# Kernel optimization log

Measured on AMD Instinct MI355X. Metric: run time of the kernel, lower is better.

The kernel has to match this reference:

```python
import jax, jax.numpy as jnp
import numpy as np

B, L, C = 131072, 50, 3
WIN = 10  # running std window


def setup_inputs() -> dict:
    key = jax.random.key(0)
    ks = jax.random.split(key, 12)
    def xavier(k, shape, fan_in, fan_out, gain):
        bound = gain * np.sqrt(6.0 / (fan_in + fan_out))
        return jax.random.uniform(k, shape, jnp.float32, -bound, bound)
    relu_g = np.sqrt(2.0)
    return {
        "signal": jax.random.normal(ks[0], (B, L, C), jnp.float32),
        # conv weights: (out_ch, in_ch, kernel)
        "conv1_w": xavier(ks[1], (5, 3, 3), 3 * 3, 5 * 3, relu_g),
        "conv1_b": jnp.zeros((5,), jnp.float32),
        "conv2_w": xavier(ks[2], (10, 5, 3), 5 * 3, 10 * 3, relu_g),
        "conv2_b": jnp.zeros((10,), jnp.float32),
        "fc1_w": xavier(ks[3], (256, 360), 360, 256, relu_g),
        "fc1_b": jnp.zeros((256,), jnp.float32),
        "fc2_w": xavier(ks[4], (64, 256), 256, 64, relu_g),
        "fc2_b": jnp.zeros((64,), jnp.float32),
        "pamap_w": xavier(ks[5], (12, 64), 64, 12, 1.0),
        "pamap_b": jnp.zeros((12,), jnp.float32),
    }


def running_std(x, w):
    # x: (B, L, C) -> (B, L - w, C); unbiased std (ddof=1) over sliding window,
    # computed with prefix sums instead of per-window kernels.
    b, l, c = x.shape
    z = jnp.zeros((b, 1, c), x.dtype)
    cs = jnp.concatenate([z, jnp.cumsum(x, axis=1)], axis=1)
    cs2 = jnp.concatenate([z, jnp.cumsum(x * x, axis=1)], axis=1)
    lo = l - w  # note: torch loop produces L - w windows (last window dropped)
    s = cs[:, w:w + lo] - cs[:, :lo]
    s2 = cs2[:, w:w + lo] - cs2[:, :lo]
    var = (s2 - s * s / w) / (w - 1)
    return jnp.sqrt(jnp.maximum(var, 0.0))


def conv1d(x, w, b):
    # x: (B, C, T), w: (O, I, K)
    y = jax.lax.conv_general_dilated(x, w, (1,), 'VALID',
                                     dimension_numbers=('NCH', 'OIH', 'NCH'))
    return y + b[None, :, None]


def reference(signal, conv1_w, conv1_b, conv2_w, conv2_b,
              fc1_w, fc1_b, fc2_w, fc2_b, pamap_w, pamap_b):
    sd = running_std(signal, WIN)            # (B, 40, 3)
    x = jnp.transpose(sd, (0, 2, 1))          # (B, 3, 40)
    h = jax.nn.relu(conv1d(x, conv1_w, conv1_b))   # (B, 5, 38)
    h = jax.nn.relu(conv1d(h, conv2_w, conv2_b))   # (B, 10, 36)
    flat = jnp.transpose(h, (0, 2, 1)).reshape(-1, 36 * 10)  # (B, 360)
    f = jax.nn.relu(flat @ fc1_w.T + fc1_b)
    f = jax.nn.relu(f @ fc2_w.T + fc2_b)
    logits = f @ pamap_w.T + pamap_b           # flag=False -> pamap head
    return jax.nn.log_softmax(logits, axis=1)
```

## Files before the change

kernel.cpp:

```cpp
#include <hip/hip_runtime.h>
#include <hip/hip_bf16.h>

typedef __attribute__((ext_vector_type(8))) short bf16x8;
typedef __attribute__((ext_vector_type(4))) float f32x4;
typedef __attribute__((ext_vector_type(8))) unsigned short u16x8;

static __device__ __forceinline__ unsigned short bf16bits(float v) {
    __hip_bfloat16 h = __float2bfloat16(v);
    return *(unsigned short*)&h;
}

__global__ __launch_bounds__(256) void prep_weights(
    const float* __restrict__ fc1w, const float* __restrict__ fc2w,
    __hip_bfloat16* __restrict__ w1o, __hip_bfloat16* __restrict__ w2o)
{
    int id = blockIdx.x * 256 + threadIdx.x;
    if (id < 256 * 384) {
        int n = id / 384, k2 = id - n * 384;
        float v = 0.0f;
        if (k2 < 360) {
            int o = k2 / 36, t = k2 - o * 36;
            v = fc1w[n * 360 + t * 10 + o];
        }
        w1o[id] = __float2bfloat16(v);
    } else {
        int id2 = id - 256 * 384;
        if (id2 < 64 * 256) w2o[id2] = __float2bfloat16(fc2w[id2]);
    }
}

__global__ __launch_bounds__(256, 8) void features_kernel(
    const float* __restrict__ sig,
    const float* __restrict__ c1w_g, const float* __restrict__ c1b_g,
    const float* __restrict__ c2w_g, const float* __restrict__ c2b_g,
    __hip_bfloat16* __restrict__ Fg)
{
    __shared__ __align__(16) unsigned char smem[16648];
    float* Sraw = (float*)smem;
    float* SD   = (float*)(smem + 4800);
    float* C1   = (float*)(smem + 9408);
    float* cw   = (float*)(smem + 15808);

    const int tid = threadIdx.x;
    const int blk = blockIdx.x;

    {
        const float4* gs = (const float4*)(sig + (size_t)blk * 1200);
        float4* ls = (float4*)Sraw;
        for (int i = tid; i < 300; i += 256) ls[i] = gs[i];
        if (tid < 210) {
            float v;
            if (tid < 45)       v = c1w_g[tid];
            else if (tid < 50)  v = c1b_g[tid - 45];
            else if (tid < 200) v = c2w_g[tid - 50];
            else                v = c2b_g[tid - 200];
            cw[tid] = v;
        }
    }
    __syncthreads();

    if (tid < 192) {
        int s = tid / 24, r = tid - s * 24;
        int c = r >> 3, q = r & 7;
        const float* p = Sraw + s * 150 + c + q * 15;
        float x[14];
        #pragma unroll
        for (int j = 0; j < 14; ++j) x[j] = p[j * 3];
        float sum = 0.f, sq = 0.f;
        #pragma unroll
        for (int j = 0; j < 10; ++j) { sum += x[j]; sq += x[j] * x[j]; }
        float* o = SD + (s * 3 + c) * 48 + q * 5;
        #pragma unroll
        for (int i = 0; i < 5; ++i) {
            float var = (sq - sum * sum * 0.1f) * (1.0f / 9.0f);
            o[i] = sqrtf(fmaxf(var, 0.f));
            if (i < 4) {
                float d = x[i + 10] - x[i];
                sq  += d * (x[i + 10] + x[i]);
                sum += d;
            }
        }
    }
    __syncthreads();

    for (int id = tid; id < 400; id += 256) {
        int s = id / 50, r = id - s * 50;
        int o = r / 10, tq = r - o * 10;
        int t0 = tq * 4;
        float b = cw[45 + o];
        float a0 = b, a1 = b, a2 = b, a3 = b;
        #pragma unroll
        for (int ci = 0; ci < 3; ++ci) {
            const float* row = SD + (s * 3 + ci) * 48 + t0;
            float4 ya = *(const float4*)row;
            float4 yb = *(const float4*)(row + 4);
            float w0 = cw[o * 9 + ci * 3 + 0];
            float w1 = cw[o * 9 + ci * 3 + 1];
            float w2 = cw[o * 9 + ci * 3 + 2];
            a0 += w0 * ya.x + w1 * ya.y + w2 * ya.z;
            a1 += w0 * ya.y + w1 * ya.z + w2 * ya.w;
            a2 += w0 * ya.z + w1 * ya.w + w2 * yb.x;
            a3 += w0 * ya.w + w1 * yb.x + w2 * yb.y;
        }
        float* dst = C1 + (s * 5 + o) * 40 + t0;
        if (tq < 9) {
            float4 v = {fmaxf(a0, 0.f), fmaxf(a1, 0.f), fmaxf(a2, 0.f), fmaxf(a3, 0.f)};
            *(float4*)dst = v;
        } else {
            dst[0] = fmaxf(a0, 0.f);
            dst[1] = fmaxf(a1, 0.f);
        }
    }
    __syncthreads();

    if (tid < 96) {
        int s = tid / 12, j = tid - s * 12;
        *(unsigned int*)(smem + s * 768 + 720 + 4 * j) = 0u;
    }
    for (int id = tid; id < 720; id += 256) {
        int s = id / 90, r = id - s * 90;
        int o = r / 9, tq = r - o * 9;
        int t0 = tq * 4;
        float b = cw[200 + o];
        float a0 = b, a1 = b, a2 = b, a3 = b;
        #pragma unroll
        for (int i2 = 0; i2 < 5; ++i2) {
            const float* row = C1 + (s * 5 + i2) * 40 + t0;
            float4 ya = *(const float4*)row;
            float4 yb = *(const float4*)(row + 4);
            float w0 = cw[50 + o * 15 + i2 * 3 + 0];
            float w1 = cw[50 + o * 15 + i2 * 3 + 1];
            float w2 = cw[50 + o * 15 + i2 * 3 + 2];
            a0 += w0 * ya.x + w1 * ya.y + w2 * ya.z;
            a1 += w0 * ya.y + w1 * ya.z + w2 * ya.w;
            a2 += w0 * ya.z + w1 * ya.w + w2 * yb.x;
            a3 += w0 * ya.w + w1 * yb.x + w2 * yb.y;
        }
        unsigned int p0 = (unsigned int)bf16bits(fmaxf(a0, 0.f))
                        | ((unsigned int)bf16bits(fmaxf(a1, 0.f)) << 16);
        unsigned int p1 = (unsigned int)bf16bits(fmaxf(a2, 0.f))
                        | ((unsigned int)bf16bits(fmaxf(a3, 0.f)) << 16);
        uint2 pk = {p0, p1};
        *(uint2*)(smem + s * 768 + (o * 36 + t0) * 2) = pk;
    }
    __syncthreads();

    {
        const u16x8* srcv = (const u16x8*)smem;
        u16x8* dstv = (u16x8*)Fg + (size_t)blk * 384;
        for (int i = tid; i < 384; i += 256) dstv[i] = srcv[i];
    }
}

__global__ __launch_bounds__(256, 2) void fc_head_kernel(
    const __hip_bfloat16* __restrict__ Fg,
    const __hip_bfloat16* __restrict__ W1, const __hip_bfloat16* __restrict__ W2,
    const float* __restrict__ fc1b, const float* __restrict__ fc2b,
    const float* __restrict__ pw, const float* __restrict__ pb,
    float* __restrict__ out)
{
    __shared__ __align__(16) unsigned char smem[63536];
    float* pwl = (float*)(smem + 60416);
    float* pbl = (float*)(smem + 63488);

    const int tid  = threadIdx.x;
    const int blk  = blockIdx.x;
    const int w    = tid >> 6;
    const int lane = tid & 63;
    const int ml   = lane & 15;
    const int kg   = lane >> 4;
    unsigned char* Tw = smem + 50176 + w * 2560;

    for (int i = tid; i < 780; i += 256) {
        if (i < 768) pwl[i] = pw[i]; else pbl[i - 768] = pb[i - 768];
    }

    const __hip_bfloat16* myF = Fg + (size_t)(blk * 128 + w * 32 + ml) * 384;
    bf16x8 bfr[12][2];
    #pragma unroll
    for (int kk = 0; kk < 12; ++kk) {
        bfr[kk][0] = *(const bf16x8*)(myF + kk * 32 + kg * 8);
        bfr[kk][1] = *(const bf16x8*)(myF + 16 * 384 + kk * 32 + kg * 8);
    }

    {
        const u16x8* src = (const u16x8*)W1;
        __hip_bfloat16* b0 = (__hip_bfloat16*)smem;
        #pragma unroll
        for (int it = 0; it < 6; ++it) {
            int v = tid + it * 256;
            int n = v / 48, k8 = v - n * 48;
            *(u16x8*)(b0 + n * 392 + k8 * 8) = src[v];
        }
    }

    f32x4 acc2[4][2];
    #pragma unroll
    for (int t2 = 0; t2 < 4; ++t2) {
        acc2[t2][0] = f32x4{0, 0, 0, 0};
        acc2[t2][1] = f32x4{0, 0, 0, 0};
    }

    for (int c = 0; c < 8; ++c) {
        __syncthreads();
        const __hip_bfloat16* cur = (const __hip_bfloat16*)(smem + (c & 1) * 25088);

        u16x8 nf[6];
        if (c < 7) {
            const u16x8* src = (const u16x8*)(W1 + (c + 1) * 32 * 384);
            #pragma unroll
            for (int it = 0; it < 6; ++it) nf[it] = src[tid + it * 256];
        }

        f32x4 a1acc[2][2];
        #pragma unroll
        for (int rt = 0; rt < 2; ++rt) {
            a1acc[rt][0] = f32x4{0, 0, 0, 0};
            a1acc[rt][1] = f32x4{0, 0, 0, 0};
        }
        #pragma unroll
        for (int kk = 0; kk < 12; ++kk) {
            bf16x8 w0 = *(const bf16x8*)(cur + ml * 392 + kk * 32 + kg * 8);
            bf16x8 w1 = *(const bf16x8*)(cur + (16 + ml) * 392 + kk * 32 + kg * 8);
            a1acc[0][0] = __builtin_amdgcn_mfma_f32_16x16x32_bf16(w0, bfr[kk][0], a1acc[0][0], 0, 0, 0);
            a1acc[0][1] = __builtin_amdgcn_mfma_f32_16x16x32_bf16(w0, bfr[kk][1], a1acc[0][1], 0, 0, 0);
            a1acc[1][0] = __builtin_amdgcn_mfma_f32_16x16x32_bf16(w1, bfr[kk][0], a1acc[1][0], 0, 0, 0);
            a1acc[1][1] = __builtin_amdgcn_mfma_f32_16x16x32_bf16(w1, bfr[kk][1], a1acc[1][1], 0, 0, 0);
        }

        #pragma unroll
        for (int rt = 0; rt < 2; ++rt) {
            float4 b4 = *(const float4*)(fc1b + c * 32 + rt * 16 + kg * 4);
            #pragma unroll
            for (int st = 0; st < 2; ++st) {
                unsigned int p0 =
                    (unsigned int)bf16bits(fmaxf(a1acc[rt][st][0] + b4.x, 0.f))
                  | ((unsigned int)bf16bits(fmaxf(a1acc[rt][st][1] + b4.y, 0.f)) << 16);
                unsigned int p1 =
                    (unsigned int)bf16bits(fmaxf(a1acc[rt][st][2] + b4.z, 0.f))
                  | ((unsigned int)bf16bits(fmaxf(a1acc[rt][st][3] + b4.w, 0.f)) << 16);
                uint2 pk = {p0, p1};
                *(uint2*)(Tw + (st * 16 + ml) * 80 + (rt * 16 + kg * 4) * 2) = pk;
            }
        }
        asm volatile("s_waitcnt lgkmcnt(0)" ::: "memory");
        __builtin_amdgcn_sched_barrier(0);

        bf16x8 pf0 = *(const bf16x8*)(Tw + ml * 80 + kg * 16);
        bf16x8 pf1 = *(const bf16x8*)(Tw + (16 + ml) * 80 + kg * 16);
        #pragma unroll
        for (int t2 = 0; t2 < 4; ++t2) {
            bf16x8 a2 = *(const bf16x8*)(W2 + (t2 * 16 + ml) * 256 + c * 32 + kg * 8);
            acc2[t2][0] = __builtin_amdgcn_mfma_f32_16x16x32_bf16(a2, pf0, acc2[t2][0], 0, 0, 0);
            acc2[t2][1] = __builtin_amdgcn_mfma_f32_16x16x32_bf16(a2, pf1, acc2[t2][1], 0, 0, 0);
        }

        if (c < 7) {
            __hip_bfloat16* nxt = (__hip_bfloat16*)(smem + ((c + 1) & 1) * 25088);
            #pragma unroll
            for (int it = 0; it < 6; ++it) {
                int v = tid + it * 256;
                int n = v / 48, k8 = v - n * 48;
                *(u16x8*)(nxt + n * 392 + k8 * 8) = nf[it];
            }
        }
    }

    #pragma unroll
    for (int st = 0; st < 2; ++st) {
        float h[16];
        #pragma unroll
        for (int t2 = 0; t2 < 4; ++t2) {
            float4 b4 = *(const float4*)(fc2b + t2 * 16 + kg * 4);
            #pragma unroll
            for (int i = 0; i < 4; ++i)
                h[t2 * 4 + i] = fmaxf(acc2[t2][st][i] + ((const float*)&b4)[i], 0.f);
        }
        float lg[12];
        #pragma unroll
        for (int j = 0; j < 12; ++j) {
            float s = 0.f;
            #pragma unroll
            for (int t2 = 0; t2 < 4; ++t2) {
                float4 wv = *(const float4*)(pwl + j * 64 + t2 * 16 + kg * 4);
                s += wv.x * h[t2 * 4 + 0] + wv.y * h[t2 * 4 + 1]
                   + wv.z * h[t2 * 4 + 2] + wv.w * h[t2 * 4 + 3];
            }
            lg[j] = s;
        }
        #pragma unroll
        for (int j = 0; j < 12; ++j) {
            lg[j] += __shfl_xor(lg[j], 16);
            lg[j] += __shfl_xor(lg[j], 32);
            lg[j] += pbl[j];
        }
        float m = lg[0];
        #pragma unroll
        for (int j = 1; j < 12; ++j) m = fmaxf(m, lg[j]);
        float e = 0.f;
        #pragma unroll
        for (int j = 0; j < 12; ++j) e += __expf(lg[j] - m);
        float lse = m + __logf(e);
        if (kg == 0) {
            float* op = out + (size_t)(blk * 128 + w * 32 + st * 16 + ml) * 12;
            float4 o0 = {lg[0] - lse, lg[1] - lse, lg[2]  - lse, lg[3]  - lse};
            float4 o1 = {lg[4] - lse, lg[5] - lse, lg[6]  - lse, lg[7]  - lse};
            float4 o2 = {lg[8] - lse, lg[9] - lse, lg[10] - lse, lg[11] - lse};
            ((float4*)op)[0] = o0; ((float4*)op)[1] = o1; ((float4*)op)[2] = o2;
        }
    }
}

extern "C" void kernel_launch(void* const* d_in, const int* in_sizes, int n_in,
                              void* d_out, int out_size, void* d_ws, size_t ws_size,
                              hipStream_t stream) {
    const float* sig = (const float*)d_in[0];
    const float* c1w = (const float*)d_in[1];
    const float* c1b = (const float*)d_in[2];
    const float* c2w = (const float*)d_in[3];
    const float* c2b = (const float*)d_in[4];
    const float* f1w = (const float*)d_in[5];
    const float* f1b = (const float*)d_in[6];
    const float* f2w = (const float*)d_in[7];
    const float* f2b = (const float*)d_in[8];
    const float* pw  = (const float*)d_in[9];
    const float* pb  = (const float*)d_in[10];
    float* out = (float*)d_out;

    __hip_bfloat16* W1 = (__hip_bfloat16*)d_ws;
    __hip_bfloat16* W2 = (__hip_bfloat16*)((char*)d_ws + 196608);
    __hip_bfloat16* Fg = (__hip_bfloat16*)((char*)d_ws + 229376);

    prep_weights<<<448, 256, 0, stream>>>(f1w, f2w, W1, W2);
    features_kernel<<<16384, 256, 0, stream>>>(sig, c1w, c1b, c2w, c2b, Fg);
    fc_head_kernel<<<1024, 256, 0, stream>>>(Fg, W1, W2, f1b, f2b, pw, pb, out);
}
```

Measured before the change: 245.2 us.

## Run conv layers on MFMA with 32 samples per block; prefetch W2 fragments

The features kernel now handles 32 samples per block instead of 8. It reads the signal straight from global memory into registers to compute the running std, stores it as bf16, and computes both conv1d layers as im2col-style 16x16x32 bf16 MFMAs with padded shared-memory tiles. This replaces the scalar FMA loops. The fc head also prefetches the next W2 A-fragments into registers one chunk ahead. The gains come from removing scalar conv work and raising per-block throughput. The costs are lower occupancy from larger LDS, uncoalesced strided global reads of the signal, and bf16 rounding of the intermediate features.

```diff
diff --git a/kernel.cpp b/kernel.cpp
--- a/kernel.cpp
+++ b/kernel.cpp
@@ -29,25 +29,35 @@
     }
 }
 
-__global__ __launch_bounds__(256, 8) void features_kernel(
+#define P_BASE  0
+#define P_TILE  10496
+#define P_SSTR  656
+#define SD_BASE 20992
+#define SD_TILE 11008
+#define SD_SSTR 688
+#define F_BASE  20992
+#define F_RSTR  784
+#define CW_OFF  46080
+__global__ __launch_bounds__(256, 3) void features_kernel(
     const float* __restrict__ sig,
     const float* __restrict__ c1w_g, const float* __restrict__ c1b_g,
     const float* __restrict__ c2w_g, const float* __restrict__ c2b_g,
     __hip_bfloat16* __restrict__ Fg)
 {
-    __shared__ __align__(16) unsigned char smem[16648];
-    float* Sraw = (float*)smem;
-    float* SD   = (float*)(smem + 4800);
-    float* C1   = (float*)(smem + 9408);
-    float* cw   = (float*)(smem + 15808);
-
-    const int tid = threadIdx.x;
-    const int blk = blockIdx.x;
-
-    {
-        const float4* gs = (const float4*)(sig + (size_t)blk * 1200);
-        float4* ls = (float4*)Sraw;
-        for (int i = tid; i < 300; i += 256) ls[i] = gs[i];
+    __shared__ __align__(16) unsigned char smem[46920];
+    float* cw = (float*)(smem + CW_OFF);
+
+    const int tid  = threadIdx.x;
+    const int blk  = blockIdx.x;
+    const int wv   = tid >> 6;
+    const int lane = tid & 63;
+    const int ml   = lane & 15;
+    const int kg   = lane >> 4;
+
+    {
+        f32x4 z = {0.f, 0.f, 0.f, 0.f};
+        for (int i = tid; i < 2688; i += 256)
+            *(f32x4*)(smem + i * 16) = z;
         if (tid < 210) {
             float v;
             if (tid < 45)       v = c1w_g[tid];
@@ -60,95 +70,95 @@
     __syncthreads();
 
     if (tid < 192) {
-        int s = tid / 24, r = tid - s * 24;
-        int c = r >> 3, q = r & 7;
-        const float* p = Sraw + s * 150 + c + q * 15;
-        float x[14];
-        #pragma unroll
-        for (int j = 0; j < 14; ++j) x[j] = p[j * 3];
+        int s = tid / 6, r = tid - s * 6;
+        int c = r >> 1, h = r & 1;
+        int j0 = h * 20;
+        const float* g = sig + (size_t)blk * 4800 + s * 150 + c;
+        float x[30];
+        #pragma unroll
+        for (int j = 0; j < 30; ++j) x[j] = g[(j0 + j) * 3];
         float sum = 0.f, sq = 0.f;
         #pragma unroll
         for (int j = 0; j < 10; ++j) { sum += x[j]; sq += x[j] * x[j]; }
-        float* o = SD + (s * 3 + c) * 48 + q * 5;
-        #pragma unroll
-        for (int i = 0; i < 5; ++i) {
+        unsigned char* sd = smem + SD_BASE + (s >> 4) * SD_TILE + (s & 15) * SD_SSTR + c * 2;
+        #pragma unroll
+        for (int i = 0; i < 20; ++i) {
             float var = (sq - sum * sum * 0.1f) * (1.0f / 9.0f);
-            o[i] = sqrtf(fmaxf(var, 0.f));
-            if (i < 4) {
+            *(unsigned short*)(sd + (j0 + i) * 16) = bf16bits(sqrtf(fmaxf(var, 0.f)));
+            if (i < 19) {
                 float d = x[i + 10] - x[i];
                 sq  += d * (x[i + 10] + x[i]);
                 sum += d;
             }
         }
     }
+
+    bf16x8 B1f, B2f;
+    #pragma unroll
+    for (int j = 0; j < 8; ++j) {
+        float v1 = (ml < 5  && kg < 3 && j < 3) ? cw[ml * 9 + j * 3 + kg] : 0.f;
+        float v2 = (ml < 10 && kg < 3 && j < 5) ? cw[50 + ml * 15 + j * 3 + kg] : 0.f;
+        B1f[j] = (short)bf16bits(v1);
+        B2f[j] = (short)bf16bits(v2);
+    }
+    const float c1bias = (ml < 5)  ? cw[45 + ml]  : 0.f;
+    const float c2bias = (ml < 10) ? cw[200 + ml] : 0.f;
     __syncthreads();
 
-    for (int id = tid; id < 400; id += 256) {
-        int s = id / 50, r = id - s * 50;
-        int o = r / 10, tq = r - o * 10;
-        int t0 = tq * 4;
-        float b = cw[45 + o];
-        float a0 = b, a1 = b, a2 = b, a3 = b;
-        #pragma unroll
-        for (int ci = 0; ci < 3; ++ci) {
-            const float* row = SD + (s * 3 + ci) * 48 + t0;
-            float4 ya = *(const float4*)row;
-            float4 yb = *(const float4*)(row + 4);
-            float w0 = cw[o * 9 + ci * 3 + 0];
-            float w1 = cw[o * 9 + ci * 3 + 1];
-            float w2 = cw[o * 9 + ci * 3 + 2];
-            a0 += w0 * ya.x + w1 * ya.y + w2 * ya.z;
-            a1 += w0 * ya.y + w1 * ya.z + w2 * ya.w;
-            a2 += w0 * ya.z + w1 * ya.w + w2 * yb.x;
-            a3 += w0 * ya.w + w1 * yb.x + w2 * yb.y;
-        }
-        float* dst = C1 + (s * 5 + o) * 40 + t0;
-        if (tq < 9) {
-            float4 v = {fmaxf(a0, 0.f), fmaxf(a1, 0.f), fmaxf(a2, 0.f), fmaxf(a3, 0.f)};
-            *(float4*)dst = v;
-        } else {
-            dst[0] = fmaxf(a0, 0.f);
-            dst[1] = fmaxf(a1, 0.f);
+    {
+        const int tile = wv >> 1, half = wv & 1;
+        const unsigned char* sdb = smem + SD_BASE + tile * SD_TILE + ml * SD_SSTR;
+        unsigned char* pb = smem + P_BASE + tile * P_TILE + ml * 2;
+        #pragma unroll
+        for (int it = 0; it < 19; ++it) {
+            int t = half * 19 + it;
+            bf16x8 a = *(const bf16x8*)(sdb + (t + kg) * 16);
+            f32x4 acc = {0.f, 0.f, 0.f, 0.f};
+            acc = __builtin_amdgcn_mfma_f32_16x16x32_bf16(a, B1f, acc, 0, 0, 0);
+            if (ml < 5) {
+                #pragma unroll
+                for (int i = 0; i < 4; ++i) {
+                    float v = fmaxf(acc[i] + c1bias, 0.f);
+                    *(unsigned short*)(pb + (kg * 4 + i) * P_SSTR + t * 16) = bf16bits(v);
+                }
+            }
         }
     }
     __syncthreads();
 
-    if (tid < 96) {
-        int s = tid / 12, j = tid - s * 12;
-        *(unsigned int*)(smem + s * 768 + 720 + 4 * j) = 0u;
-    }
-    for (int id = tid; id < 720; id += 256) {
-        int s = id / 90, r = id - s * 90;
-        int o = r / 9, tq = r - o * 9;
-        int t0 = tq * 4;
-        float b = cw[200 + o];
-        float a0 = b, a1 = b, a2 = b, a3 = b;
-        #pragma unroll
-        for (int i2 = 0; i2 < 5; ++i2) {
-            const float* row = C1 + (s * 5 + i2) * 40 + t0;
-            float4 ya = *(const float4*)row;
-            float4 yb = *(const float4*)(row + 4);
-            float w0 = cw[50 + o * 15 + i2 * 3 + 0];
-            float w1 = cw[50 + o * 15 + i2 * 3 + 1];
-            float w2 = cw[50 + o * 15 + i2 * 3 + 2];
-            a0 += w0 * ya.x + w1 * ya.y + w2 * ya.z;
-            a1 += w0 * ya.y + w1 * ya.z + w2 * ya.w;
-            a2 += w0 * ya.z + w1 * ya.w + w2 * yb.x;
-            a3 += w0 * ya.w + w1 * yb.x + w2 * yb.y;
-        }
-        unsigned int p0 = (unsigned int)bf16bits(fmaxf(a0, 0.f))
-                        | ((unsigned int)bf16bits(fmaxf(a1, 0.f)) << 16);
-        unsigned int p1 = (unsigned int)bf16bits(fmaxf(a2, 0.f))
-                        | ((unsigned int)bf16bits(fmaxf(a3, 0.f)) << 16);
-        uint2 pk = {p0, p1};
-        *(uint2*)(smem + s * 768 + (o * 36 + t0) * 2) = pk;
+    if (tid < 128) {
+        f32x4 z = {0.f, 0.f, 0.f, 0.f};
+        int r = tid >> 2, q = tid & 3;
+        *(f32x4*)(smem + F_BASE + r * F_RSTR + 720 + q * 16) = z;
+    }
+
+    {
+        const int tile = wv >> 1, half = wv & 1;
+        const unsigned char* pbr = smem + P_BASE + tile * P_TILE + ml * P_SSTR;
+        unsigned char* fb = smem + F_BASE + tile * 16 * F_RSTR + ml * 72;
+        #pragma unroll
+        for (int it = 0; it < 18; ++it) {
+            int t = half * 18 + it;
+            bf16x8 a = *(const bf16x8*)(pbr + (t + kg) * 16);
+            f32x4 acc = {0.f, 0.f, 0.f, 0.f};
+            acc = __builtin_amdgcn_mfma_f32_16x16x32_bf16(a, B2f, acc, 0, 0, 0);
+            if (ml < 10) {
+                #pragma unroll
+                for (int i = 0; i < 4; ++i) {
+                    float v = fmaxf(acc[i] + c2bias, 0.f);
+                    *(unsigned short*)(fb + (kg * 4 + i) * F_RSTR + t * 2) = bf16bits(v);
+                }
+            }
+        }
     }
     __syncthreads();
 
     {
-        const u16x8* srcv = (const u16x8*)smem;
-        u16x8* dstv = (u16x8*)Fg + (size_t)blk * 384;
-        for (int i = tid; i < 384; i += 256) dstv[i] = srcv[i];
+        u16x8* dstv = (u16x8*)Fg + (size_t)blk * 1536;
+        for (int i = tid; i < 1536; i += 256) {
+            int r = i / 48, cc = i - r * 48;
+            dstv[i] = *(const u16x8*)(smem + F_BASE + r * F_RSTR + cc * 16);
+        }
     }
 }
 
@@ -193,6 +203,10 @@
             *(u16x8*)(b0 + n * 392 + k8 * 8) = src[v];
         }
     }
+    bf16x8 a2f[4];
+    #pragma unroll
+    for (int t2 = 0; t2 < 4; ++t2)
+        a2f[t2] = *(const bf16x8*)(W2 + (t2 * 16 + ml) * 256 + kg * 8);
 
     f32x4 acc2[4][2];
     #pragma unroll
@@ -206,10 +220,14 @@
         const __hip_bfloat16* cur = (const __hip_bfloat16*)(smem + (c & 1) * 25088);
 
         u16x8 nf[6];
+        bf16x8 a2n[4];
         if (c < 7) {
             const u16x8* src = (const u16x8*)(W1 + (c + 1) * 32 * 384);
             #pragma unroll
             for (int it = 0; it < 6; ++it) nf[it] = src[tid + it * 256];
+            #pragma unroll
+            for (int t2 = 0; t2 < 4; ++t2)
+                a2n[t2] = *(const bf16x8*)(W2 + (t2 * 16 + ml) * 256 + (c + 1) * 32 + kg * 8);
         }
 
         f32x4 a1acc[2][2];
@@ -250,9 +268,8 @@
         bf16x8 pf1 = *(const bf16x8*)(Tw + (16 + ml) * 80 + kg * 16);
         #pragma unroll
         for (int t2 = 0; t2 < 4; ++t2) {
-            bf16x8 a2 = *(const bf16x8*)(W2 + (t2 * 16 + ml) * 256 + c * 32 + kg * 8);
-            acc2[t2][0] = __builtin_amdgcn_mfma_f32_16x16x32_bf16(a2, pf0, acc2[t2][0], 0, 0, 0);
-            acc2[t2][1] = __builtin_amdgcn_mfma_f32_16x16x32_bf16(a2, pf1, acc2[t2][1], 0, 0, 0);
+            acc2[t2][0] = __builtin_amdgcn_mfma_f32_16x16x32_bf16(a2f[t2], pf0, acc2[t2][0], 0, 0, 0);
+            acc2[t2][1] = __builtin_amdgcn_mfma_f32_16x16x32_bf16(a2f[t2], pf1, acc2[t2][1], 0, 0, 0);
         }
 
         if (c < 7) {
@@ -263,6 +280,8 @@
                 int n = v / 48, k8 = v - n * 48;
                 *(u16x8*)(nxt + n * 392 + k8 * 8) = nf[it];
             }
+            #pragma unroll
+            for (int t2 = 0; t2 < 4; ++t2) a2f[t2] = a2n[t2];
         }
     }
 
@@ -282,9 +301,9 @@
             float s = 0.f;
             #pragma unroll
             for (int t2 = 0; t2 < 4; ++t2) {
-                float4 wv = *(const float4*)(pwl + j * 64 + t2 * 16 + kg * 4);
-                s += wv.x * h[t2 * 4 + 0] + wv.y * h[t2 * 4 + 1]
-                   + wv.z * h[t2 * 4 + 2] + wv.w * h[t2 * 4 + 3];
+                float4 wv4 = *(const float4*)(pwl + j * 64 + t2 * 16 + kg * 4);
+                s += wv4.x * h[t2 * 4 + 0] + wv4.y * h[t2 * 4 + 1]
+                   + wv4.z * h[t2 * 4 + 2] + wv4.w * h[t2 * 4 + 3];
             }
             lg[j] = s;
         }
@@ -332,6 +351,6 @@
     __hip_bfloat16* Fg = (__hip_bfloat16*)((char*)d_ws + 229376);
 
     prep_weights<<<448, 256, 0, stream>>>(f1w, f2w, W1, W2);
-    features_kernel<<<16384, 256, 0, stream>>>(sig, c1w, c1b, c2w, c2b, Fg);
+    features_kernel<<<4096, 256, 0, stream>>>(sig, c1w, c1b, c2w, c2b, Fg);
     fc_head_kernel<<<1024, 256, 0, stream>>>(Fg, W1, W2, f1b, f2b, pw, pb, out);
 }
```

Result: faster. 219.8 us (-10.4%).
